# Kernel optimization log

Hardware: AMD Instinct MI355X
Metric: run time of the kernel (lower is better)

Reference implementation:

```python
import jax, jax.numpy as jnp
import numpy as np

B_SZ, SEQ, D_MODEL = 2, 512, 1024
EXPAND, HEAD_DIM = 2, 64
D_INNER = EXPAND * D_MODEL            # 2048
N_HEADS = D_INNER // HEAD_DIM         # 32
D_STATE = 64
EPS = 1e-6
PROJ_DIM = 2 * D_INNER + 2 * N_HEADS * D_STATE + N_HEADS  # 8224


def setup_inputs() -> dict:
    key = jax.random.key(0)
    k = jax.random.split(key, 5)
    return {
        "hidden": jax.random.normal(k[0], (B_SZ, SEQ, D_MODEL), jnp.float32),
        "W_in": 0.02 * jax.random.normal(k[1], (D_MODEL, PROJ_DIM), jnp.float32),
        "dt_bias": 0.5 * jax.random.normal(k[2], (N_HEADS,), jnp.float32),
        "A_log": 0.5 * jax.random.normal(k[3], (N_HEADS,), jnp.float32),
        "norm_weight": jnp.ones((D_INNER,), jnp.float32),
        "W_out": 0.02 * jax.random.normal(k[4], (D_INNER, D_MODEL), jnp.float32),
    }


def _rope(x, theta):
    # x: [b,l,h,n] interleaved pairs (view_as_complex convention); theta: [b,l,h,n//2]
    x0, x1 = x[..., 0::2], x[..., 1::2]
    c, s = jnp.cos(theta), jnp.sin(theta)
    y = jnp.stack([x0 * c - x1 * s, x0 * s + x1 * c], axis=-1)
    return y.reshape(x.shape)


def reference(hidden, W_in, dt_bias, A_log, norm_weight, W_out):
    b, l, _ = hidden.shape
    proj = hidden @ W_in  # [b,l,PROJ_DIM]
    hn = N_HEADS * D_STATE
    z = proj[..., :D_INNER]
    xr = proj[..., D_INNER:2 * D_INNER].reshape(b, l, N_HEADS, HEAD_DIM)
    Bm = proj[..., 2 * D_INNER:2 * D_INNER + hn].reshape(b, l, N_HEADS, D_STATE)
    Cm = proj[..., 2 * D_INNER + hn:2 * D_INNER + 2 * hn].reshape(b, l, N_HEADS, D_STATE)
    dt = jax.nn.softplus(proj[..., -N_HEADS:] + dt_bias)  # [b,l,h]

    A = -jnp.exp(A_log)                 # [h], negative decay
    alpha = jnp.exp(dt * A)             # decay factor
    beta = 0.5 * dt * alpha             # trapezoidal: half-step on previous input
    gamma = 0.5 * dt                    # trapezoidal: half-step on current input

    # data-dependent RoPE: phase is cumulative dt scaled by per-dim inverse freq
    half = D_STATE // 2
    inv_freq = 1.0 / (10000.0 ** (jnp.arange(half, dtype=jnp.float32) / half))
    theta = jnp.cumsum(dt, axis=1)[..., None] * inv_freq  # [b,l,h,half]
    Bm = _rope(Bm, theta)
    Cm = _rope(Cm, theta)

    # shifted (t-1) inputs, zero at t=0 (h starts at 0 so alpha-at-t0 is a no-op)
    Bp = jnp.pad(Bm[:, :-1], ((0, 0), (1, 0), (0, 0), (0, 0)))
    xp = jnp.pad(xr[:, :-1], ((0, 0), (1, 0), (0, 0), (0, 0)))

    tl = lambda t: jnp.moveaxis(t, 1, 0)  # time-major for scan
    xs = (tl(xr), tl(Bm), tl(Cm), tl(Bp), tl(xp), tl(alpha), tl(beta), tl(gamma))
    h0 = jnp.zeros((b, N_HEADS, D_STATE, HEAD_DIM), hidden.dtype)

    def step(h, inp):
        x_t, B_t, C_t, Bprev, xprev, a, bt, g = inp
        h = (a[..., None, None] * h
             + bt[..., None, None] * jnp.einsum('bhn,bhp->bhnp', Bprev, xprev)
             + g[..., None, None] * jnp.einsum('bhn,bhp->bhnp', B_t, x_t))
        y = jnp.einsum('bhn,bhnp->bhp', C_t, h)
        return h, y

    _, ys = jax.lax.scan(step, h0, xs)          # ys: [l,b,h,p]
    y = jnp.moveaxis(ys, 0, 1).reshape(b, l, D_INNER)

    y = y * jax.nn.silu(z)                      # gated output
    rms = jnp.sqrt(jnp.mean(y * y, axis=-1, keepdims=True) + EPS)
    y = y / rms * norm_weight                   # RMSNorm
    return y @ W_out
```

## Files before the change

kernel.cpp:

```cpp
#include <hip/hip_runtime.h>
#include <stdint.h>

typedef __attribute__((ext_vector_type(8))) short short8;
typedef __attribute__((ext_vector_type(8))) unsigned short ushort8;
typedef __attribute__((ext_vector_type(4))) unsigned short usv4;
typedef __attribute__((ext_vector_type(4))) float float4v;

#define B_SZ 2
#define SEQ 512
#define D_MODEL 1024
#define D_INNER 2048
#define N_HEADS 32
#define HEAD_DIM 64
#define D_STATE 64
#define PROJ_DIM 8224
#define NPAD 8320
#define MROWS 1024

__device__ __forceinline__ unsigned short f2bf(float f) {
    unsigned u = __builtin_bit_cast(unsigned, f);
    u += 0x7fffu + ((u >> 16) & 1u);
    return (unsigned short)(u >> 16);
}
__device__ __forceinline__ float bf2f(unsigned short h) {
    return __builtin_bit_cast(float, (unsigned)h << 16);
}

__device__ __forceinline__ void gld16(unsigned short* lds, const unsigned short* g) {
#if __has_builtin(__builtin_amdgcn_global_load_lds)
    __builtin_amdgcn_global_load_lds(
        (const __attribute__((address_space(1))) void*)g,
        (__attribute__((address_space(3))) void*)lds, 16, 0, 0);
#else
    *(short8*)lds = *(const short8*)g;
#endif
}

__device__ void transpose_body(const float* __restrict__ src,
                               unsigned short* __restrict__ dst,
                               int R, int C, int bx, int by, float* T, int tid) {
    int c0 = bx * 64, r0 = by * 64;
    int row = tid >> 2, cg = (tid & 3) * 16;
    #pragma unroll
    for (int k = 0; k < 4; k++) {
        int col = cg + k * 4;
        float4v v;
        if (c0 + col + 3 < C) {
            v = *(const float4v*)&src[(size_t)(r0 + row) * C + c0 + col];
        } else {
            #pragma unroll
            for (int e = 0; e < 4; e++)
                v[e] = (c0 + col + e < C) ? src[(size_t)(r0 + row) * C + c0 + col + e] : 0.f;
        }
        *(float4v*)&T[row * 68 + col] = v;
    }
    __syncthreads();
    int drow = tid >> 2, sg = (tid & 3) * 16;
    ushort8 v[2];
    #pragma unroll
    for (int k = 0; k < 16; k++) v[k >> 3][k & 7] = f2bf(T[(sg + k) * 68 + drow]);
    unsigned short* d = &dst[(size_t)(c0 + drow) * R + r0 + sg];
    *(ushort8*)&d[0] = v[0];
    *(ushort8*)&d[8] = v[1];
}

__global__ __launch_bounds__(256) void prep_fat(
    const float* __restrict__ hidden, const float* __restrict__ W_in,
    const float* __restrict__ W_out, unsigned short* __restrict__ Hb,
    unsigned short* __restrict__ Wt1, unsigned short* __restrict__ Wt2) {
    __shared__ float T[64 * 68];
    int blk = blockIdx.x, tid = threadIdx.x;
    if (blk < 1024) {
        int i = blk * 1024 + tid * 4;
        float4v v = *(const float4v*)&hidden[i];
        usv4 o;
        #pragma unroll
        for (int k = 0; k < 4; k++) o[k] = f2bf(v[k]);
        *(usv4*)&Hb[i] = o;
    } else if (blk < 3104) {
        int q = blk - 1024;
        transpose_body(W_in, Wt1, D_MODEL, PROJ_DIM, q % 130, q / 130, T, tid);
    } else {
        int q = blk - 3104;
        transpose_body(W_out, Wt2, D_INNER, D_MODEL, q % 16, q / 16, T, tid);
    }
}

template <bool BF16OUT>
__global__ __launch_bounds__(256) void gemm_bt(
    const unsigned short* __restrict__ A, const unsigned short* __restrict__ Bt,
    void* __restrict__ Cout, int M, int N, int K, int klen) {
    __shared__ unsigned short As[8192];
    __shared__ unsigned short Bs[8192];
    int tid = threadIdx.x;
    int lane = tid & 63, w = tid >> 6, quad = lane >> 4, l15 = lane & 15;
    int m0 = blockIdx.y * 128, n0 = blockIdx.x * 128;
    int kb = blockIdx.z * klen, ke = kb + klen;
    int wm = (w & 1) * 64, wn = (w >> 1) * 64;
    float4v acc[4][4];
    #pragma unroll
    for (int i = 0; i < 4; i++)
        #pragma unroll
        for (int j = 0; j < 4; j++) acc[i][j] = (float4v){0.f, 0.f, 0.f, 0.f};

    int rs = tid >> 3;
    int gl = ((tid & 7) ^ (rs & 7)) * 8;
    const unsigned short* ap = &A [(size_t)(m0 + rs) * K + gl];
    const unsigned short* bp = &Bt[(size_t)(n0 + rs) * K + gl];
    int rx = l15 & 7;

    for (int k0 = kb; k0 < ke; k0 += 64) {
        __syncthreads();
        #pragma unroll
        for (int p = 0; p < 4; p++) {
            gld16(&As[p * 2048 + tid * 8], ap + (size_t)(p * 32) * K + k0);
            gld16(&Bs[p * 2048 + tid * 8], bp + (size_t)(p * 32) * K + k0);
        }
        __syncthreads();
        #pragma unroll
        for (int kq = 0; kq < 2; kq++) {
            short8 af[4], bfr[4];
            #pragma unroll
            for (int mt = 0; mt < 4; mt++)
                af[mt] = *(const short8*)&As[(wm + mt * 16 + l15) * 64 + (((kq << 2) + quad) ^ rx) * 8];
            #pragma unroll
            for (int nt = 0; nt < 4; nt++)
                bfr[nt] = *(const short8*)&Bs[(wn + nt * 16 + l15) * 64 + (((kq << 2) + quad) ^ rx) * 8];
            #pragma unroll
            for (int mt = 0; mt < 4; mt++)
                #pragma unroll
                for (int nt = 0; nt < 4; nt++)
                    acc[mt][nt] = __builtin_amdgcn_mfma_f32_16x16x32_bf16(
                        af[mt], bfr[nt], acc[mt][nt], 0, 0, 0);
        }
    }
    #pragma unroll
    for (int mt = 0; mt < 4; mt++)
        #pragma unroll
        for (int nt = 0; nt < 4; nt++)
            #pragma unroll
            for (int r = 0; r < 4; r++) {
                int row = m0 + wm + mt * 16 + quad * 4 + r;
                int col = n0 + wn + nt * 16 + l15;
                if (col < N) {
                    if (BF16OUT)
                        ((unsigned short*)Cout)[(size_t)blockIdx.z * M * N + (size_t)row * N + col]
                            = f2bf(acc[mt][nt][r]);
                    else
                        ((float*)Cout)[(size_t)blockIdx.z * M * N + (size_t)row * N + col]
                            = acc[mt][nt][r];
                }
            }
}

__global__ __launch_bounds__(256) void reduce4(
    const float* __restrict__ P, float* __restrict__ out, int n) {
    int i = (blockIdx.x * 256 + threadIdx.x) * 4;
    float4v s = *(const float4v*)&P[i];
    #pragma unroll
    for (int z = 1; z < 4; z++) {
        float4v v = *(const float4v*)&P[(size_t)z * n + i];
        #pragma unroll
        for (int k = 0; k < 4; k++) s[k] += v[k];
    }
    *(float4v*)&out[i] = s;
}

__global__ __launch_bounds__(256) void dt_scan(
    const unsigned short* __restrict__ proj, const float* __restrict__ dt_bias,
    float* __restrict__ dt_arr, float* __restrict__ cum_arr) {
    __shared__ float chs[8];
    int bh = blockIdx.x;
    int b = bh >> 5, h = bh & 31;
    int tid = threadIdx.x, lane = tid & 63, w = tid >> 6;
    float bias = dt_bias[h];
    int t0 = w * 64 + lane, t1 = 256 + w * 64 + lane;
    float raw0 = bf2f(proj[(size_t)(b * SEQ + t0) * PROJ_DIM + 8192 + h]) + bias;
    float raw1 = bf2f(proj[(size_t)(b * SEQ + t1) * PROJ_DIM + 8192 + h]) + bias;
    float dt0 = raw0 > 20.f ? raw0 : log1pf(expf(raw0));
    float dt1 = raw1 > 20.f ? raw1 : log1pf(expf(raw1));
    float v0 = dt0, v1 = dt1;
    #pragma unroll
    for (int d = 1; d < 64; d <<= 1) {
        float n0 = __shfl_up(v0, d, 64);
        float n1 = __shfl_up(v1, d, 64);
        if (lane >= d) { v0 += n0; v1 += n1; }
    }
    if (lane == 63) { chs[w] = v0; chs[4 + w] = v1; }
    __syncthreads();
    float off0 = 0.f, off1 = 0.f;
    #pragma unroll
    for (int c = 0; c < 8; c++) {
        float s = chs[c];
        if (c < w) off0 += s;
        if (c < 4 + w) off1 += s;
    }
    dt_arr[bh * SEQ + t0] = dt0;  cum_arr[bh * SEQ + t0] = off0 + v0;
    dt_arr[bh * SEQ + t1] = dt1;  cum_arr[bh * SEQ + t1] = off1 + v1;
}

__global__ __launch_bounds__(256) void pack_fat(
    const unsigned short* __restrict__ proj, const float* __restrict__ cum_arr,
    unsigned short* __restrict__ Bh, unsigned short* __restrict__ Ch,
    unsigned short* __restrict__ Xt) {
    __shared__ unsigned short XT[64 * 72];
    int blk = blockIdx.x, tid = threadIdx.x;
    if (blk < 1024) {
        int m = blk, b = m >> 9, t = m & 511;
        const float k_l2 = 13.287712379549449f / 32.f;
        #pragma unroll
        for (int i = 0; i < 4; i++) {
            int q = i * 256 + tid;
            int h = q >> 5, j = q & 31;
            float cum = cum_arr[(b * 32 + h) * SEQ + t];
            float th = cum * exp2f(-(float)j * k_l2);
            float s, c;
            __sincosf(th, &s, &c);
            size_t rb = (size_t)m * PROJ_DIM;
            unsigned bu = *(const unsigned*)&proj[rb + 4096 + h * 64 + 2 * j];
            unsigned cu = *(const unsigned*)&proj[rb + 6144 + h * 64 + 2 * j];
            float b0 = bf2f((unsigned short)(bu & 0xffff)), b1 = bf2f((unsigned short)(bu >> 16));
            float c0 = bf2f((unsigned short)(cu & 0xffff)), c1 = bf2f((unsigned short)(cu >> 16));
            size_t dst = ((size_t)(b * 32 + h) * SEQ + t) * 64 + 2 * j;
            unsigned ob = (unsigned)f2bf(b0 * c - b1 * s) | ((unsigned)f2bf(b0 * s + b1 * c) << 16);
            unsigned oc = (unsigned)f2bf(c0 * c - c1 * s) | ((unsigned)f2bf(c0 * s + c1 * c) << 16);
            *(unsigned*)&Bh[dst] = ob;
            *(unsigned*)&Ch[dst] = oc;
        }
    } else {
        int q = blk - 1024;
        int bh = q >> 3, s0 = (q & 7) * 64;
        int b = bh >> 5, h = bh & 31;
        int r = tid >> 2, cg = (tid & 3) * 16;
        const unsigned short* src = &proj[(size_t)(b * SEQ + s0 + r) * PROJ_DIM + 2048 + h * 64 + cg];
        *(ushort8*)&XT[r * 72 + cg]     = *(const ushort8*)&src[0];
        *(ushort8*)&XT[r * 72 + cg + 8] = *(const ushort8*)&src[8];
        __syncthreads();
        int p = tid >> 2, sg = (tid & 3) * 16;
        ushort8 v[2];
        #pragma unroll
        for (int k = 0; k < 16; k++) v[k >> 3][k & 7] = XT[(sg + k) * 72 + p];
        unsigned short* dst = &Xt[((size_t)bh * 64 + p) * SEQ + s0 + sg];
        *(ushort8*)&dst[0] = v[0];
        *(ushort8*)&dst[8] = v[1];
    }
}

__global__ __launch_bounds__(256) void attn_scan(
    const unsigned short* __restrict__ Bh, const unsigned short* __restrict__ Ch,
    const unsigned short* __restrict__ Xt, const float* __restrict__ dt_arr,
    const float* __restrict__ cum_arr, const float* __restrict__ A_log,
    float* __restrict__ y_ws) {
    __shared__ unsigned short Bs[4096];
    __shared__ unsigned short Xs[4096];
    __shared__ unsigned short Ps[4096];
    int qt = blockIdx.x, bh = blockIdx.y;
    int b = bh >> 5, h = bh & 31;
    float Aneg = -expf(A_log[h]);
    int tid = threadIdx.x, lane = tid & 63, w = tid >> 6;
    int quad = lane >> 4, l15 = lane & 15;

    int qrow = qt * 64 + w * 16 + l15;
    const unsigned short* Cptr = Ch + ((size_t)bh * SEQ + qrow) * 64;
    short8 cf[2];
    cf[0] = *(const short8*)&Cptr[quad * 8];
    cf[1] = *(const short8*)&Cptr[32 + quad * 8];

    int trow[4];
    float cumt[4];
    #pragma unroll
    for (int r = 0; r < 4; r++) {
        trow[r] = qt * 64 + w * 16 + quad * 4 + r;
        cumt[r] = cum_arr[bh * SEQ + trow[r]];
    }
    float4v yacc[4];
    #pragma unroll
    for (int i = 0; i < 4; i++) yacc[i] = (float4v){0.f, 0.f, 0.f, 0.f};

    for (int st = 0; st <= qt; st++) {
        __syncthreads();
        const unsigned short* bsrc = Bh + ((size_t)bh * SEQ + st * 64) * 64;
        gld16(&Bs[tid * 8],         bsrc + tid * 8);
        gld16(&Bs[(tid + 256) * 8], bsrc + (tid + 256) * 8);
        const unsigned short* xsrc = Xt + (size_t)bh * 64 * SEQ + st * 64;
        {
            int e = tid;
            int p = e >> 3, so = (e & 7) * 8;
            gld16(&Xs[p * 64 + so], xsrc + (size_t)p * SEQ + so);
            e = tid + 256;
            p = e >> 3; so = (e & 7) * 8;
            gld16(&Xs[p * 64 + so], xsrc + (size_t)p * SEQ + so);
        }
        __syncthreads();
        float4v sacc[4];
        #pragma unroll
        for (int i = 0; i < 4; i++) sacc[i] = (float4v){0.f, 0.f, 0.f, 0.f};
        #pragma unroll
        for (int kk = 0; kk < 2; kk++)
            #pragma unroll
            for (int nt = 0; nt < 4; nt++) {
                short8 bf8 = *(const short8*)&Bs[(nt * 16 + l15) * 64 + kk * 32 + quad * 8];
                sacc[nt] = __builtin_amdgcn_mfma_f32_16x16x32_bf16(cf[kk], bf8, sacc[nt], 0, 0, 0);
            }
        #pragma unroll
        for (int nt = 0; nt < 4; nt++) {
            int s = st * 64 + nt * 16 + l15;
            float cums = cum_arr[bh * SEQ + s];
            float dts = dt_arr[bh * SEQ + s];
            float dts1 = (s + 1 < SEQ) ? dt_arr[bh * SEQ + s + 1] : 0.f;
            #pragma unroll
            for (int r = 0; r < 4; r++) {
                int t = trow[r];
                float wgt = (s > t) ? 0.f
                          : expf(Aneg * (cumt[r] - cums)) * 0.5f * (dts + ((s < t) ? dts1 : 0.f));
                Ps[w * 1024 + (quad * 4 + r) * 64 + nt * 16 + l15] = f2bf(sacc[nt][r] * wgt);
            }
        }
        __syncthreads();
        #pragma unroll
        for (int kk = 0; kk < 2; kk++) {
            short8 af = *(const short8*)&Ps[w * 1024 + l15 * 64 + kk * 32 + quad * 8];
            #pragma unroll
            for (int pt = 0; pt < 4; pt++) {
                short8 xf = *(const short8*)&Xs[(pt * 16 + l15) * 64 + kk * 32 + quad * 8];
                yacc[pt] = __builtin_amdgcn_mfma_f32_16x16x32_bf16(af, xf, yacc[pt], 0, 0, 0);
            }
        }
    }
    #pragma unroll
    for (int pt = 0; pt < 4; pt++)
        #pragma unroll
        for (int r = 0; r < 4; r++) {
            int t = trow[r];
            int p = pt * 16 + l15;
            y_ws[((size_t)b * SEQ + t) * D_INNER + h * 64 + p] = yacc[pt][r];
        }
}

__global__ __launch_bounds__(256) void gated_rmsnorm(
    const float* __restrict__ y_ws, const unsigned short* __restrict__ proj,
    const float* __restrict__ nw, unsigned short* __restrict__ Y2) {
    __shared__ float red[4];
    int m = blockIdx.x, tid = threadIdx.x;
    const float* yrow = y_ws + (size_t)m * D_INNER;
    const unsigned short* zrow = proj + (size_t)m * PROJ_DIM;
    int j0 = tid * 8;
    ushort8 zv = *(const ushort8*)&zrow[j0];
    float v[8];
    float ss = 0.f;
    #pragma unroll
    for (int k = 0; k < 8; k++) {
        float y = yrow[j0 + k];
        float z = bf2f(zv[k]);
        float g = y * (z / (1.f + expf(-z)));
        v[k] = g;
        ss += g * g;
    }
    #pragma unroll
    for (int d = 32; d > 0; d >>= 1) ss += __shfl_down(ss, d, 64);
    if ((tid & 63) == 0) red[tid >> 6] = ss;
    __syncthreads();
    float tot = red[0] + red[1] + red[2] + red[3];
    float inv = 1.0f / sqrtf(tot / (float)D_INNER + 1e-6f);
    #pragma unroll
    for (int k = 0; k < 8; k++)
        Y2[(size_t)m * D_INNER + j0 + k] = f2bf(v[k] * inv * nw[j0 + k]);
}


extern "C" void kernel_launch(void* const* d_in, const int* in_sizes, int n_in,
                              void* d_out, int out_size, void* d_ws, size_t ws_size,
                              hipStream_t stream) {
    const float* hidden   = (const float*)d_in[0];
    const float* W_in     = (const float*)d_in[1];
    const float* dt_bias  = (const float*)d_in[2];
    const float* A_log    = (const float*)d_in[3];
    const float* norm_w   = (const float*)d_in[4];
    const float* W_out    = (const float*)d_in[5];
    float* out = (float*)d_out;

    char* ws = (char*)d_ws;
    unsigned short* Wt1  = (unsigned short*)(ws);
    unsigned short* Hb   = (unsigned short*)(ws + 17039360);
    unsigned short* proj = (unsigned short*)(ws + 19136512);
    float* dt_arr        = (float*)(ws + 35979264);
    float* cum_arr       = (float*)(ws + 36110336);
    unsigned short* Bh   = (unsigned short*)(ws + 36241408);
    unsigned short* Ch   = (unsigned short*)(ws + 40435712);
    unsigned short* Xt   = (unsigned short*)(ws + 44630016);
    float* y_ws          = (float*)(ws + 48824320);
    unsigned short* Y2   = (unsigned short*)(ws + 57212928);
    unsigned short* Wt2  = (unsigned short*)(ws + 61407232);
    float* Pk = (float*)proj;

    prep_fat<<<3616, 256, 0, stream>>>(hidden, W_in, W_out, Hb, Wt1, Wt2);
    gemm_bt<true><<<dim3(NPAD / 128, MROWS / 128, 1), 256, 0, stream>>>(
        Hb, Wt1, proj, MROWS, PROJ_DIM, D_MODEL, D_MODEL);
    dt_scan<<<64, 256, 0, stream>>>(proj, dt_bias, dt_arr, cum_arr);
    pack_fat<<<1536, 256, 0, stream>>>(proj, cum_arr, Bh, Ch, Xt);
    attn_scan<<<dim3(8, 64), 256, 0, stream>>>(Bh, Ch, Xt, dt_arr, cum_arr, A_log, y_ws);
    gated_rmsnorm<<<MROWS, 256, 0, stream>>>(y_ws, proj, norm_w, Y2);
    gemm_bt<false><<<dim3(D_MODEL / 128, MROWS / 128, 4), 256, 0, stream>>>(
        Y2, Wt2, Pk, MROWS, D_MODEL, D_INNER, D_INNER / 4);
    reduce4<<<MROWS * D_MODEL / 1024, 256, 0, stream>>>(Pk, out, MROWS * D_MODEL);
}
```

Measured before the change: 194.5 us.

## Double-buffer GEMM shared tiles and store scan output as bf16

The bf16 GEMM now keeps two LDS buffers per operand. It issues the global-to-LDS loads for the next k-tile before computing the current one, which drops one barrier per iteration and overlaps load latency with MFMA work. Separately, the scan kernel writes its output as bf16 rather than fp32, and the gated RMSNorm reads it back with vector loads, halving that intermediate's traffic. Workspace offsets are shifted to match. The costs are doubled LDS use (64KB per block), which may reduce occupancy, and some extra rounding error in the intermediate y.

```diff
diff --git a/kernel.cpp b/kernel.cpp
--- a/kernel.cpp
+++ b/kernel.cpp
@@ -90,8 +90,8 @@
 __global__ __launch_bounds__(256) void gemm_bt(
     const unsigned short* __restrict__ A, const unsigned short* __restrict__ Bt,
     void* __restrict__ Cout, int M, int N, int K, int klen) {
-    __shared__ unsigned short As[8192];
-    __shared__ unsigned short Bs[8192];
+    __shared__ unsigned short As[2][8192];
+    __shared__ unsigned short Bs[2][8192];
     int tid = threadIdx.x;
     int lane = tid & 63, w = tid >> 6, quad = lane >> 4, l15 = lane & 15;
     int m0 = blockIdx.y * 128, n0 = blockIdx.x * 128;
@@ -109,23 +109,32 @@
     const unsigned short* bp = &Bt[(size_t)(n0 + rs) * K + gl];
     int rx = l15 & 7;
 
+    #pragma unroll
+    for (int p = 0; p < 4; p++) {
+        gld16(&As[0][p * 2048 + tid * 8], ap + (size_t)(p * 32) * K + kb);
+        gld16(&Bs[0][p * 2048 + tid * 8], bp + (size_t)(p * 32) * K + kb);
+    }
+    __syncthreads();
+
+    int cur = 0;
     for (int k0 = kb; k0 < ke; k0 += 64) {
-        __syncthreads();
-        #pragma unroll
-        for (int p = 0; p < 4; p++) {
-            gld16(&As[p * 2048 + tid * 8], ap + (size_t)(p * 32) * K + k0);
-            gld16(&Bs[p * 2048 + tid * 8], bp + (size_t)(p * 32) * K + k0);
-        }
-        __syncthreads();
+        int nxt = cur ^ 1;
+        if (k0 + 64 < ke) {
+            #pragma unroll
+            for (int p = 0; p < 4; p++) {
+                gld16(&As[nxt][p * 2048 + tid * 8], ap + (size_t)(p * 32) * K + k0 + 64);
+                gld16(&Bs[nxt][p * 2048 + tid * 8], bp + (size_t)(p * 32) * K + k0 + 64);
+            }
+        }
         #pragma unroll
         for (int kq = 0; kq < 2; kq++) {
             short8 af[4], bfr[4];
             #pragma unroll
             for (int mt = 0; mt < 4; mt++)
-                af[mt] = *(const short8*)&As[(wm + mt * 16 + l15) * 64 + (((kq << 2) + quad) ^ rx) * 8];
+                af[mt] = *(const short8*)&As[cur][(wm + mt * 16 + l15) * 64 + (((kq << 2) + quad) ^ rx) * 8];
             #pragma unroll
             for (int nt = 0; nt < 4; nt++)
-                bfr[nt] = *(const short8*)&Bs[(wn + nt * 16 + l15) * 64 + (((kq << 2) + quad) ^ rx) * 8];
+                bfr[nt] = *(const short8*)&Bs[cur][(wn + nt * 16 + l15) * 64 + (((kq << 2) + quad) ^ rx) * 8];
             #pragma unroll
             for (int mt = 0; mt < 4; mt++)
                 #pragma unroll
@@ -133,6 +142,8 @@
                     acc[mt][nt] = __builtin_amdgcn_mfma_f32_16x16x32_bf16(
                         af[mt], bfr[nt], acc[mt][nt], 0, 0, 0);
         }
+        __syncthreads();
+        cur = nxt;
     }
     #pragma unroll
     for (int mt = 0; mt < 4; mt++)
@@ -250,7 +261,7 @@
     const unsigned short* __restrict__ Bh, const unsigned short* __restrict__ Ch,
     const unsigned short* __restrict__ Xt, const float* __restrict__ dt_arr,
     const float* __restrict__ cum_arr, const float* __restrict__ A_log,
-    float* __restrict__ y_ws) {
+    unsigned short* __restrict__ y_ws) {
     __shared__ unsigned short Bs[4096];
     __shared__ unsigned short Xs[4096];
     __shared__ unsigned short Ps[4096];
@@ -333,24 +344,25 @@
         for (int r = 0; r < 4; r++) {
             int t = trow[r];
             int p = pt * 16 + l15;
-            y_ws[((size_t)b * SEQ + t) * D_INNER + h * 64 + p] = yacc[pt][r];
+            y_ws[((size_t)b * SEQ + t) * D_INNER + h * 64 + p] = f2bf(yacc[pt][r]);
         }
 }
 
 __global__ __launch_bounds__(256) void gated_rmsnorm(
-    const float* __restrict__ y_ws, const unsigned short* __restrict__ proj,
+    const unsigned short* __restrict__ y_ws, const unsigned short* __restrict__ proj,
     const float* __restrict__ nw, unsigned short* __restrict__ Y2) {
     __shared__ float red[4];
     int m = blockIdx.x, tid = threadIdx.x;
-    const float* yrow = y_ws + (size_t)m * D_INNER;
+    const unsigned short* yrow = y_ws + (size_t)m * D_INNER;
     const unsigned short* zrow = proj + (size_t)m * PROJ_DIM;
     int j0 = tid * 8;
+    ushort8 yv = *(const ushort8*)&yrow[j0];
     ushort8 zv = *(const ushort8*)&zrow[j0];
     float v[8];
     float ss = 0.f;
     #pragma unroll
     for (int k = 0; k < 8; k++) {
-        float y = yrow[j0 + k];
+        float y = bf2f(yv[k]);
         float z = bf2f(zv[k]);
         float g = y * (z / (1.f + expf(-z)));
         v[k] = g;
@@ -388,9 +400,9 @@
     unsigned short* Bh   = (unsigned short*)(ws + 36241408);
     unsigned short* Ch   = (unsigned short*)(ws + 40435712);
     unsigned short* Xt   = (unsigned short*)(ws + 44630016);
-    float* y_ws          = (float*)(ws + 48824320);
-    unsigned short* Y2   = (unsigned short*)(ws + 57212928);
-    unsigned short* Wt2  = (unsigned short*)(ws + 61407232);
+    unsigned short* y_ws = (unsigned short*)(ws + 48824320);
+    unsigned short* Y2   = (unsigned short*)(ws + 53018624);
+    unsigned short* Wt2  = (unsigned short*)(ws + 57212928);
     float* Pk = (float*)proj;
 
     prep_fat<<<3616, 256, 0, stream>>>(hidden, W_in, W_out, Hb, Wt1, Wt2);
```

Result: slower. 202.7 us (+4.2%).
